# Kernel tuning notes

Measured on AMD Instinct MI355X. Metric: run time of the kernel, lower is better.

The kernel has to match this reference:

```python
import jax, jax.numpy as jnp
import numpy as np

NEG_SLOPE_ATT = 0.2   # GATConv attention leaky relu
NEG_SLOPE_ACT = 0.01  # F.leaky_relu default between layers


def gat_conv(x, src, dst, W, att_src, att_dst, bias, num_nodes):
    """PyG GATConv (concat=True, self-loops already in src/dst, no dropout at eval)."""
    H, C = att_src.shape
    h = (x @ W).reshape(num_nodes, H, C)            # [N,H,C]
    a_src = jnp.einsum('nhc,hc->nh', h, att_src)    # [N,H]
    a_dst = jnp.einsum('nhc,hc->nh', h, att_dst)
    e = jax.nn.leaky_relu(a_src[src] + a_dst[dst], NEG_SLOPE_ATT)  # [E,H]
    # segment softmax over incoming edges of each dst node
    m = jax.ops.segment_max(e, dst, num_segments=num_nodes)
    e = jnp.exp(e - m[dst])
    s = jax.ops.segment_sum(e, dst, num_segments=num_nodes)
    alpha = e / (s[dst] + 1e-16)                    # [E,H]
    msg = h[src] * alpha[..., None]                 # [E,H,C]
    out = jax.ops.segment_sum(msg, dst, num_segments=num_nodes)
    return out.reshape(num_nodes, H * C) + bias


def setup_inputs() -> dict:
    key = jax.random.key(0)
    ks = jax.random.split(key, 16)
    N, E = 50000, 1600000
    in_dim, hidden, heads, out_dim = 128, 32, 4, 64

    def glorot(k, shape):
        fan = shape[0] + shape[-1]
        return jax.random.uniform(k, shape, jnp.float32, -1.0, 1.0) * np.sqrt(6.0 / fan)

    x = jax.random.normal(ks[0], (N, in_dim), jnp.float32)
    edge_index = jax.random.randint(ks[1], (2, E), 0, N, jnp.int64)
    return {
        'x': x,
        'edge_index': edge_index,
        'W1': glorot(ks[2], (in_dim, heads * hidden)),
        'a1_src': glorot(ks[3], (heads, hidden)),
        'a1_dst': glorot(ks[4], (heads, hidden)),
        'b1': jnp.zeros((heads * hidden,), jnp.float32),
        'W2': glorot(ks[5], (heads * hidden, out_dim)),
        'a2_src': glorot(ks[6], (1, out_dim)),
        'a2_dst': glorot(ks[7], (1, out_dim)),
        'b2': jnp.zeros((out_dim,), jnp.float32),
        'Wd1': glorot(ks[8], (2 * out_dim, hidden)),
        'bd1': jnp.zeros((hidden,), jnp.float32),
        'Wd2': glorot(ks[9], (hidden, 1)),
        'bd2': jnp.zeros((1,), jnp.float32),
    }


def reference(x, edge_index, W1, a1_src, a1_dst, b1, W2, a2_src, a2_dst, b2,
              Wd1, bd1, Wd2, bd2):
    N = x.shape[0]
    # GATConv adds self-loops internally
    loops = jnp.arange(N, dtype=edge_index.dtype)
    src = jnp.concatenate([edge_index[0], loops])
    dst = jnp.concatenate([edge_index[1], loops])

    h1 = gat_conv(x, src, dst, W1, a1_src, a1_dst, b1, N)
    h1 = jax.nn.leaky_relu(h1, NEG_SLOPE_ACT)
    z = gat_conv(h1, src, dst, W2, a2_src, a2_dst, b2, N)

    # decoder: gather-concat-MLP over original edges
    feats = jnp.concatenate([z[edge_index[0]], z[edge_index[1]]], axis=1)  # [E,2*out]
    hdec = jax.nn.relu(feats @ Wd1 + bd1)
    edge_pred = hdec @ Wd2 + bd2                                           # [E,1]
    return edge_pred, z
```

## Files before the change

### kernel.cpp

```cpp
#include <hip/hip_runtime.h>
#include <hip/hip_bf16.h>
#include <math.h>

#define NEG_ATT 0.2f
#define NEG_ACT 0.01f
#define SHIFT_C 16.0f
#define CHUNK_E 8192
#define STAGE_MAX 12544

typedef __hip_bfloat16  bf16;
typedef unsigned short u16;
typedef short s8v __attribute__((ext_vector_type(8)));
typedef float f4v __attribute__((ext_vector_type(4)));

__device__ __forceinline__ float bflo(unsigned w) { return __uint_as_float(w << 16); }
__device__ __forceinline__ float bfhi(unsigned w) { return __uint_as_float(w & 0xFFFF0000u); }
__device__ __forceinline__ float lrelu_att(float a) { return fmaxf(a, NEG_ATT * a); }
__device__ __forceinline__ u16 f2b(float v) { bf16 h = __float2bfloat16(v); return *(u16*)&h; }

template<int MODE, int K, int CT, int INBF>
__device__ __forceinline__ void mfma_body(int bx, const void* __restrict__ in_,
                                          const u16* __restrict__ Wp,
                                          const float* __restrict__ bias,
                                          bf16* __restrict__ ob, bf16* __restrict__ ob2,
                                          float* __restrict__ o1, float* __restrict__ o2, int N) {
    constexpr int KK = K / 32;
    constexpr int KP = K + 8;
    __shared__ u16 As[64][KP];
    const int tid = threadIdx.x;
    const int w = tid >> 6, lane = tid & 63;
    const int row0 = bx * 64;
    for (int i = tid; i < 64 * K; i += 256) {
        int rl = (K == 128) ? (i >> 7) : (i >> 6);
        int k  = i - rl * K;
        int n = row0 + rl;
        float v = 0.f;
        if (n < N) {
            if (INBF) v = __uint_as_float((unsigned)((const u16*)in_)[(size_t)n * K + k] << 16);
            else      v = ((const float*)in_)[(size_t)n * K + k];
        }
        if (MODE == 1) v = v > 0.f ? v : NEG_ACT * v;
        As[rl][k] = f2b(v);
    }
    __syncthreads();
    const int rloc = w * 16 + (lane & 15);
    const int kgrp = lane >> 4;
    s8v af[KK];
    #pragma unroll
    for (int kk = 0; kk < KK; ++kk)
        af[kk] = *(const s8v*)&As[rloc][kk * 32 + kgrp * 8];
    #pragma unroll
    for (int ct = 0; ct < CT; ++ct) {
        f4v acc = {0.f, 0.f, 0.f, 0.f};
        #pragma unroll
        for (int kk = 0; kk < KK; ++kk) {
            s8v b = *(const s8v*)&Wp[(size_t)((ct * KK + kk) * 64 + lane) * 8];
            acc = __builtin_amdgcn_mfma_f32_16x16x32_bf16(af[kk], b, acc, 0, 0, 0);
        }
        const int colb = ct * 16 + (lane & 15);
        #pragma unroll
        for (int r = 0; r < 4; ++r) {
            int n = row0 + w * 16 + kgrp * 4 + r;
            if (n >= N) continue;
            float val = acc[r];
            if (MODE == 0) {
                if (colb < 128)      ob[(size_t)n * 128 + colb] = __float2bfloat16(val);
                else if (colb < 132) o1[n * 4 + (colb - 128)] = val;
                else if (colb < 136) o2[n * 4 + (colb - 132)] = val;
            } else if (MODE == 1) {
                if (colb < 64)       ob[(size_t)n * 64 + colb] = __float2bfloat16(val);
                else if (colb == 64) o1[n] = val;
                else if (colb == 65) o2[n] = val;
            } else {
                if (colb < 32) ob[(size_t)n * 32 + colb] = __float2bfloat16(val + bias[colb]);
                else           ob2[(size_t)n * 32 + (colb - 32)] = __float2bfloat16(val);
            }
        }
    }
}

template<int MODE, int K, int CT, int INBF>
__global__ void k_mfma(const void* __restrict__ in_, const u16* __restrict__ Wp,
                       const float* __restrict__ bias,
                       bf16* __restrict__ ob, bf16* __restrict__ ob2,
                       float* __restrict__ o1, float* __restrict__ o2, int N) {
    mfma_body<MODE, K, CT, INBF>(blockIdx.x, in_, Wp, bias, ob, ob2, o1, o2, N);
}

__global__ void k_packz(const float* __restrict__ W1, const float* __restrict__ a1sw,
                        const float* __restrict__ a1dw,
                        const float* __restrict__ W2, const float* __restrict__ a2sw,
                        const float* __restrict__ a2dw,
                        const float* __restrict__ Wd1,
                        u16* __restrict__ Wp1, u16* __restrict__ Wp2, u16* __restrict__ Wpd,
                        int* __restrict__ bhist) {
    if (blockIdx.x == 48) {
        if (threadIdx.x < 257) bhist[threadIdx.x] = 0;
        return;
    }
    const int T1 = 9 * 4 * 64 * 8, T2 = 5 * 4 * 64 * 8, TD = 4 * 2 * 64 * 8;
    for (int gi = blockIdx.x * 256 + threadIdx.x; gi < T1 + T2 + TD; gi += 48 * 256) {
        if (gi < T1) {
            int i = gi;
            int ct = i >> 11, rem = i & 2047;
            int kk = rem >> 9, l = (rem >> 3) & 63, j = i & 7;
            int k = kk * 32 + ((l >> 4) << 3) + j;
            int c = ct * 16 + (l & 15);
            float v = 0.f;
            if (c < 128) v = W1[k * 128 + c];
            else if (c < 132) {
                int h = c - 128;
                for (int q = 0; q < 32; ++q) v += W1[k * 128 + h * 32 + q] * a1sw[h * 32 + q];
            } else if (c < 136) {
                int h = c - 132;
                for (int q = 0; q < 32; ++q) v += W1[k * 128 + h * 32 + q] * a1dw[h * 32 + q];
            }
            Wp1[i] = f2b(v);
        } else if (gi < T1 + T2) {
            int i = gi - T1;
            int ct = i >> 11, rem = i & 2047;
            int kk = rem >> 9, l = (rem >> 3) & 63, j = i & 7;
            int k = kk * 32 + ((l >> 4) << 3) + j;
            int c = ct * 16 + (l & 15);
            float v = 0.f;
            if (c < 64) v = W2[k * 64 + c];
            else if (c == 64) { for (int q = 0; q < 64; ++q) v += W2[k * 64 + q] * a2sw[q]; }
            else if (c == 65) { for (int q = 0; q < 64; ++q) v += W2[k * 64 + q] * a2dw[q]; }
            Wp2[i] = f2b(v);
        } else {
            int i = gi - T1 - T2;
            int ct = i >> 10, rem = i & 1023;
            int kk = rem >> 9, l = (rem >> 3) & 63, j = i & 7;
            int k = kk * 32 + ((l >> 4) << 3) + j;
            int c = ct * 16 + (l & 15);
            float v = (c < 32) ? Wd1[k * 32 + c] : Wd1[(64 + k) * 32 + (c - 32)];
            Wpd[i] = f2b(v);
        }
    }
}

__global__ void k_front(const int* __restrict__ ei, int E, int N, int* __restrict__ bhist,
                        const float* __restrict__ x, const u16* __restrict__ Wp1,
                        bf16* __restrict__ h1b, float* __restrict__ a1s, float* __restrict__ a1d) {
    if (blockIdx.x < 512) {
        __shared__ int h[256];
        h[threadIdx.x] = 0;
        __syncthreads();
        const long E2 = (long)E + N;
        for (long e = (long)blockIdx.x * 256 + threadIdx.x; e < E2; e += 512L * 256) {
            int d = (e < E) ? ei[E + e] : (int)(e - E);
            atomicAdd(&h[d >> 8], 1);
        }
        __syncthreads();
        if (h[threadIdx.x]) atomicAdd(&bhist[threadIdx.x], h[threadIdx.x]);
    } else {
        mfma_body<0, 128, 9, 0>(blockIdx.x - 512, x, Wp1, nullptr, h1b, h1b, a1s, a1d, N);
    }
}

__global__ void k_scanA(const int* __restrict__ bhist, int NBKT, int total,
                        int* __restrict__ bbase, int* __restrict__ bcur,
                        int* __restrict__ rowptr, int N) {
    __shared__ int ps[256];
    const int t = threadIdx.x;
    int v = (t < NBKT) ? bhist[t] : 0;
    ps[t] = v;
    __syncthreads();
    for (int off = 1; off < 256; off <<= 1) {
        int u = (t >= off) ? ps[t - off] : 0;
        __syncthreads();
        ps[t] += u;
        __syncthreads();
    }
    int ex = ps[t] - v;
    if (t < NBKT) { bbase[t] = ex; bcur[t] = ex; }
    if (t == 0) { bbase[NBKT] = total; rowptr[N] = total; }
}

__global__ void k_scatterA(const int* __restrict__ ei, int E, int N,
                           int* __restrict__ bcur, unsigned* __restrict__ pk) {
    __shared__ int cnt[256], offs[256], cur[256], gpos[256], ps[256];
    const int tid = threadIdx.x;
    const long E2 = (long)E + N;
    const long chunk0 = (long)blockIdx.x * CHUNK_E;
    const int cmax = (int)min((long)CHUNK_E, E2 - chunk0);
    cnt[tid] = 0;
    __syncthreads();
    for (int i = tid; i < cmax; i += 256) {
        long e = chunk0 + i;
        int d = (e < E) ? ei[E + e] : (int)(e - E);
        atomicAdd(&cnt[d >> 8], 1);
    }
    __syncthreads();
    int v = cnt[tid];
    ps[tid] = v;
    __syncthreads();
    for (int off = 1; off < 256; off <<= 1) {
        int u = (tid >= off) ? ps[tid - off] : 0;
        __syncthreads();
        ps[tid] += u;
        __syncthreads();
    }
    offs[tid] = ps[tid] - v;
    cur[tid]  = ps[tid] - v;
    gpos[tid] = atomicAdd(&bcur[tid], v);
    __syncthreads();
    for (int i = tid; i < cmax; i += 256) {
        long e = chunk0 + i;
        int d, s;
        if (e < E) { d = ei[E + e]; s = ei[e]; } else { d = s = (int)(e - E); }
        int b = d >> 8;
        int r = atomicAdd(&cur[b], 1);
        pk[gpos[b] + (r - offs[b])] = ((unsigned)(d & 255) << 16) | (unsigned)s;
    }
}

__global__ void k_scatterB(const unsigned* __restrict__ pk, const int* __restrict__ bbase,
                           int N, int* __restrict__ rowptr, u16* __restrict__ col) {
    __shared__ int hist[256], loff[256], lcur[256], ps[256];
    __shared__ u16 stage[STAGE_MAX];
    const int b = blockIdx.x;
    const int tid = threadIdx.x;
    const int ebeg = bbase[b], eend = bbase[b + 1];
    const int cnt = eend - ebeg;
    hist[tid] = 0;
    __syncthreads();
    for (int i = tid; i < cnt; i += 256) {
        unsigned p = pk[ebeg + i];
        atomicAdd(&hist[(p >> 16) & 255], 1);
    }
    __syncthreads();
    int v = hist[tid];
    ps[tid] = v;
    __syncthreads();
    for (int off = 1; off < 256; off <<= 1) {
        int u = (tid >= off) ? ps[tid - off] : 0;
        __syncthreads();
        ps[tid] += u;
        __syncthreads();
    }
    loff[tid] = ps[tid] - v;
    lcur[tid] = ps[tid] - v;
    const int n0 = b << 8;
    if (n0 + tid < N) rowptr[n0 + tid] = ebeg + loff[tid];
    __syncthreads();
    if (cnt <= STAGE_MAX) {
        for (int i = tid; i < cnt; i += 256) {
            unsigned p = pk[ebeg + i];
            int r = atomicAdd(&lcur[(p >> 16) & 255], 1);
            stage[r] = (u16)(p & 0xFFFFu);
        }
        __syncthreads();
        for (int i = tid; i < cnt; i += 256) col[ebeg + i] = stage[i];
    } else {
        for (int i = tid; i < cnt; i += 256) {
            unsigned p = pk[ebeg + i];
            int r = atomicAdd(&lcur[(p >> 16) & 255], 1);
            col[ebeg + r] = (u16)(p & 0xFFFFu);
        }
    }
}

__global__ void k_aggr1(const int* __restrict__ rowptr, const u16* __restrict__ col,
                        const unsigned* __restrict__ h1q, const float* __restrict__ a1s,
                        const float* __restrict__ a1d, const float* __restrict__ b1,
                        unsigned* __restrict__ g1b, int N) {
    __shared__ float als[4][64][4];
    __shared__ int   scol[4][64];
    const int w = threadIdx.x >> 6;
    const int lane = threadIdx.x & 63;
    const int d = blockIdx.x * 4 + w;
    if (d >= N) return;
    const int lo = rowptr[d], hi = rowptr[d + 1];
    const float4 ad4 = *(const float4*)&a1d[d * 4];

    const int hh = lane >> 4;
    float acc0 = 0.f, acc1 = 0.f;
    float ws0 = 0.f, ws1 = 0.f, ws2 = 0.f, ws3 = 0.f;
    for (int base = lo; base < hi; base += 64) {
        const int cnt = min(64, hi - base);
        if (lane < cnt) {
            int s = col[base + lane];
            float4 as4 = *(const float4*)&a1s[s * 4];
            float a0 = lrelu_att(as4.x + ad4.x) - SHIFT_C;
            float a1 = lrelu_att(as4.y + ad4.y) - SHIFT_C;
            float a2 = lrelu_att(as4.z + ad4.z) - SHIFT_C;
            float a3 = lrelu_att(as4.w + ad4.w) - SHIFT_C;
            float4 al;
            al.x = __expf(a0); al.y = __expf(a1);
            al.z = __expf(a2); al.w = __expf(a3);
            ws0 += al.x; ws1 += al.y; ws2 += al.z; ws3 += al.w;
            *(float4*)&als[w][lane][0] = al;
            scol[w][lane] = s;
        }
        __builtin_amdgcn_wave_barrier();
        int t = 0;
        for (; t + 8 <= cnt; t += 8) {
            unsigned vv[8];
            float aa[8];
            #pragma unroll
            for (int q = 0; q < 8; ++q) {
                int s = scol[w][t + q];
                vv[q] = h1q[(((unsigned)s) << 6) | (unsigned)lane];
                aa[q] = als[w][t + q][hh];
            }
            #pragma unroll
            for (int q = 0; q < 8; ++q) {
                acc0 = fmaf(bflo(vv[q]), aa[q], acc0);
                acc1 = fmaf(bfhi(vv[q]), aa[q], acc1);
            }
        }
        for (; t < cnt; ++t) {
            int s = scol[w][t];
            float al = als[w][t][hh];
            unsigned v = h1q[(((unsigned)s) << 6) | (unsigned)lane];
            acc0 = fmaf(bflo(v), al, acc0);
            acc1 = fmaf(bfhi(v), al, acc1);
        }
        __builtin_amdgcn_wave_barrier();
    }
    #pragma unroll
    for (int off = 32; off >= 1; off >>= 1) {
        ws0 += __shfl_xor(ws0, off);
        ws1 += __shfl_xor(ws1, off);
        ws2 += __shfl_xor(ws2, off);
        ws3 += __shfl_xor(ws3, off);
    }
    float wsel = (hh == 0) ? ws0 : (hh == 1) ? ws1 : (hh == 2) ? ws2 : ws3;
    float inv = 1.f / (wsel + 1e-16f);
    unsigned outw = ((unsigned)f2b(acc1 * inv + b1[2 * lane + 1]) << 16)
                  | (unsigned)f2b(acc0 * inv + b1[2 * lane]);
    g1b[(size_t)d * 64 + lane] = outw;
}

__global__ void k_aggr2(const int* __restrict__ rowptr, const u16* __restrict__ col,
                        const unsigned short* __restrict__ h2s, const float* __restrict__ a2s,
                        const float* __restrict__ a2d, const float* __restrict__ b2,
                        float* __restrict__ zout, int N) {
    __shared__ float als[4][64];
    __shared__ int   scol[4][64];
    const int w = threadIdx.x >> 6;
    const int lane = threadIdx.x & 63;
    const int d = blockIdx.x * 4 + w;
    if (d >= N) return;
    const int lo = rowptr[d], hi = rowptr[d + 1];
    const float ad = a2d[d];

    float acc = 0.f, wsum = 0.f;
    for (int base = lo; base < hi; base += 64) {
        const int cnt = min(64, hi - base);
        if (lane < cnt) {
            int s = col[base + lane];
            float a = lrelu_att(a2s[s] + ad) - SHIFT_C;
            float al = __expf(a);
            wsum += al;
            als[w][lane] = al;
            scol[w][lane] = s;
        }
        __builtin_amdgcn_wave_barrier();
        int t = 0;
        for (; t + 8 <= cnt; t += 8) {
            float vv[8], aa[8];
            #pragma unroll
            for (int q = 0; q < 8; ++q) {
                int s = scol[w][t + q];
                vv[q] = __uint_as_float((unsigned)h2s[(((unsigned)s) << 6) | (unsigned)lane] << 16);
                aa[q] = als[w][t + q];
            }
            #pragma unroll
            for (int q = 0; q < 8; ++q) acc = fmaf(vv[q], aa[q], acc);
        }
        for (; t < cnt; ++t) {
            int s = scol[w][t];
            float v = __uint_as_float((unsigned)h2s[(((unsigned)s) << 6) | (unsigned)lane] << 16);
            acc = fmaf(v, als[w][t], acc);
        }
        __builtin_amdgcn_wave_barrier();
    }
    #pragma unroll
    for (int off = 32; off >= 1; off >>= 1) wsum += __shfl_xor(wsum, off);
    zout[(long)d * 64 + lane] = acc / (wsum + 1e-16f) + b2[lane];
}

__global__ void k_dec2(const int* __restrict__ ei, int E,
                       const bf16* __restrict__ u, const bf16* __restrict__ v,
                       const float* __restrict__ Wd2, const float* __restrict__ bd2,
                       float* __restrict__ pred) {
    const int g = threadIdx.x >> 3;
    const int l = threadIdx.x & 7;
    long e0 = (long)blockIdx.x * 64 + g * 2;
    if (e0 >= E) return;
    long e1 = e0 + 1;
    const bool has1 = (e1 < E);
    int s0 = ei[e0], d0 = ei[E + e0];
    int s1 = has1 ? (int)ei[e1] : s0;
    int d1 = has1 ? (int)ei[E + e1] : d0;
    uint2 ua0 = *(const uint2*)(u + (long)s0 * 32 + l * 4);
    uint2 vb0 = *(const uint2*)(v + (long)d0 * 32 + l * 4);
    uint2 ua1 = *(const uint2*)(u + (long)s1 * 32 + l * 4);
    uint2 vb1 = *(const uint2*)(v + (long)d1 * 32 + l * 4);
    float4 wv = *(const float4*)&Wd2[l * 4];
    float p0, p1;
    {
        float h0 = fmaxf(bflo(ua0.x) + bflo(vb0.x), 0.f);
        float h1 = fmaxf(bfhi(ua0.x) + bfhi(vb0.x), 0.f);
        float h2 = fmaxf(bflo(ua0.y) + bflo(vb0.y), 0.f);
        float h3 = fmaxf(bfhi(ua0.y) + bfhi(vb0.y), 0.f);
        p0 = h0 * wv.x;
        p0 = fmaf(h1, wv.y, p0);
        p0 = fmaf(h2, wv.z, p0);
        p0 = fmaf(h3, wv.w, p0);
    }
    {
        float h0 = fmaxf(bflo(ua1.x) + bflo(vb1.x), 0.f);
        float h1 = fmaxf(bfhi(ua1.x) + bfhi(vb1.x), 0.f);
        float h2 = fmaxf(bflo(ua1.y) + bflo(vb1.y), 0.f);
        float h3 = fmaxf(bfhi(ua1.y) + bfhi(vb1.y), 0.f);
        p1 = h0 * wv.x;
        p1 = fmaf(h1, wv.y, p1);
        p1 = fmaf(h2, wv.z, p1);
        p1 = fmaf(h3, wv.w, p1);
    }
    p0 += __shfl_xor(p0, 1, 8);
    p0 += __shfl_xor(p0, 2, 8);
    p0 += __shfl_xor(p0, 4, 8);
    p1 += __shfl_xor(p1, 1, 8);
    p1 += __shfl_xor(p1, 2, 8);
    p1 += __shfl_xor(p1, 4, 8);
    if (l == 0) {
        pred[e0] = p0 + bd2[0];
        if (has1) pred[e1] = p1 + bd2[0];
    }
}

extern "C" void kernel_launch(void* const* d_in, const int* in_sizes, int n_in,
                              void* d_out, int out_size, void* d_ws, size_t ws_size,
                              hipStream_t stream) {
    const float* x    = (const float*)d_in[0];
    const int*   ei   = (const int*)d_in[1];
    const float* W1   = (const float*)d_in[2];
    const float* a1sw = (const float*)d_in[3];
    const float* a1dw = (const float*)d_in[4];
    const float* b1   = (const float*)d_in[5];
    const float* W2   = (const float*)d_in[6];
    const float* a2sw = (const float*)d_in[7];
    const float* a2dw = (const float*)d_in[8];
    const float* b2   = (const float*)d_in[9];
    const float* Wd1  = (const float*)d_in[10];
    const float* bd1  = (const float*)d_in[11];
    const float* Wd2  = (const float*)d_in[12];
    const float* bd2  = (const float*)d_in[13];

    const int N = in_sizes[0] / 128;
    const int E = in_sizes[1] / 2;
    const int E2 = E + N;
    const int NBKT = (N + 255) >> 8;

    float* pred = (float*)d_out;
    float* zout = (float*)d_out + E;

    float* W = (float*)d_ws;
    size_t o = 0;
    unsigned* g1b = (unsigned*)(W + o); o += (size_t)N * 64;
    bf16* h1b  = (bf16*)(W + o); o += (size_t)N * 64;
    bf16* h2b  = (bf16*)(W + o); o += (size_t)N * 32;
    bf16* ub   = (bf16*)(W + o); o += (size_t)N * 16;
    bf16* vb   = (bf16*)(W + o); o += (size_t)N * 16;
    float* a1s = W + o; o += (size_t)N * 4;
    float* a1d = W + o; o += (size_t)N * 4;
    float* a2s = W + o; o += (size_t)N;
    float* a2d = W + o; o += (size_t)N;
    int* rowptr = (int*)(W + o); o += (size_t)N + 1;
    unsigned* pk = (unsigned*)(W + o); o += (size_t)E2;
    u16* col    = (u16*)(W + o); o += ((size_t)E2 + 1) / 2;
    int* bhist  = (int*)(W + o); o += 257;
    int* bbase  = (int*)(W + o); o += 257;
    int* bcur   = (int*)(W + o); o += 257;
    u16* Wp1   = (u16*)(W + o); o += 9216;
    u16* Wp2   = (u16*)(W + o); o += 5120;
    u16* Wpd   = (u16*)(W + o); o += 2048;
    if (ws_size < o * sizeof(float)) return;

    const int TB = 256;
    const int NBLK = (N + 63) >> 6;

    k_packz<<<49, TB, 0, stream>>>(W1, a1sw, a1dw, W2, a2sw, a2dw, Wd1, Wp1, Wp2, Wpd, bhist);
    k_front<<<512 + NBLK, TB, 0, stream>>>(ei, E, N, bhist, x, Wp1, h1b, a1s, a1d);
    k_scanA<<<1, TB, 0, stream>>>(bhist, NBKT, E2, bbase, bcur, rowptr, N);
    k_scatterA<<<(E2 + CHUNK_E - 1) / CHUNK_E, TB, 0, stream>>>(ei, E, N, bcur, pk);
    k_scatterB<<<NBKT, TB, 0, stream>>>(pk, bbase, N, rowptr, col);
    k_aggr1<<<(N + 3) / 4, TB, 0, stream>>>(rowptr, col, (const unsigned*)h1b, a1s, a1d, b1, g1b, N);
    k_mfma<1, 128, 5, 1><<<NBLK, TB, 0, stream>>>(g1b, Wp2, bd1, h2b, h2b, a2s, a2d, N);
    k_aggr2<<<(N + 3) / 4, TB, 0, stream>>>(rowptr, col, (const unsigned short*)h2b, a2s, a2d, b2, zout, N);
    k_mfma<2, 64, 4, 0><<<NBLK, TB, 0, stream>>>(zout, Wpd, bd1, ub, vb, a1s, a1d, N);
    k_dec2<<<(E + 63) / 64, TB, 0, stream>>>(ei, E, ub, vb, Wd2, bd2, pred);
}
```

Baseline: 239.4 us.

## Fuse GAT aggregation kernels with following MFMA projection GEMMs

Merges the layer-1 aggregation with the layer-2 projection GEMM, and the layer-2 aggregation with the decoder projection GEMM. Each block aggregates 64 nodes into shared memory and then runs MFMA on them. This removes the g1b intermediate buffer, the zout re-read and two kernel launches. The cost is far fewer blocks, each wave processing 16 nodes serially, which reduces parallelism and latency hiding for the irregular gathers.

```diff
diff --git a/kernel.cpp b/kernel.cpp
--- a/kernel.cpp
+++ b/kernel.cpp
@@ -18,43 +18,32 @@
 __device__ __forceinline__ float lrelu_att(float a) { return fmaxf(a, NEG_ATT * a); }
 __device__ __forceinline__ u16 f2b(float v) { bf16 h = __float2bfloat16(v); return *(u16*)&h; }
 
-template<int MODE, int K, int CT, int INBF>
-__device__ __forceinline__ void mfma_body(int bx, const void* __restrict__ in_,
-                                          const u16* __restrict__ Wp,
-                                          const float* __restrict__ bias,
-                                          bf16* __restrict__ ob, bf16* __restrict__ ob2,
-                                          float* __restrict__ o1, float* __restrict__ o2, int N) {
-    constexpr int KK = K / 32;
-    constexpr int KP = K + 8;
-    __shared__ u16 As[64][KP];
+__device__ __forceinline__ void gemm1_body(int bx, const float* __restrict__ in,
+                                           const u16* __restrict__ Wp,
+                                           bf16* __restrict__ ob,
+                                           float* __restrict__ o1, float* __restrict__ o2, int N) {
+    __shared__ u16 As[64][136];
     const int tid = threadIdx.x;
     const int w = tid >> 6, lane = tid & 63;
     const int row0 = bx * 64;
-    for (int i = tid; i < 64 * K; i += 256) {
-        int rl = (K == 128) ? (i >> 7) : (i >> 6);
-        int k  = i - rl * K;
+    for (int i = tid; i < 64 * 128; i += 256) {
+        int rl = i >> 7, k = i & 127;
         int n = row0 + rl;
-        float v = 0.f;
-        if (n < N) {
-            if (INBF) v = __uint_as_float((unsigned)((const u16*)in_)[(size_t)n * K + k] << 16);
-            else      v = ((const float*)in_)[(size_t)n * K + k];
-        }
-        if (MODE == 1) v = v > 0.f ? v : NEG_ACT * v;
-        As[rl][k] = f2b(v);
+        As[rl][k] = f2b((n < N) ? in[(size_t)n * 128 + k] : 0.f);
     }
     __syncthreads();
     const int rloc = w * 16 + (lane & 15);
     const int kgrp = lane >> 4;
-    s8v af[KK];
+    s8v af[4];
     #pragma unroll
-    for (int kk = 0; kk < KK; ++kk)
+    for (int kk = 0; kk < 4; ++kk)
         af[kk] = *(const s8v*)&As[rloc][kk * 32 + kgrp * 8];
     #pragma unroll
-    for (int ct = 0; ct < CT; ++ct) {
+    for (int ct = 0; ct < 9; ++ct) {
         f4v acc = {0.f, 0.f, 0.f, 0.f};
         #pragma unroll
-        for (int kk = 0; kk < KK; ++kk) {
-            s8v b = *(const s8v*)&Wp[(size_t)((ct * KK + kk) * 64 + lane) * 8];
+        for (int kk = 0; kk < 4; ++kk) {
+            s8v b = *(const s8v*)&Wp[(size_t)((ct * 4 + kk) * 64 + lane) * 8];
             acc = __builtin_amdgcn_mfma_f32_16x16x32_bf16(af[kk], b, acc, 0, 0, 0);
         }
         const int colb = ct * 16 + (lane & 15);
@@ -63,28 +52,11 @@
             int n = row0 + w * 16 + kgrp * 4 + r;
             if (n >= N) continue;
             float val = acc[r];
-            if (MODE == 0) {
-                if (colb < 128)      ob[(size_t)n * 128 + colb] = __float2bfloat16(val);
-                else if (colb < 132) o1[n * 4 + (colb - 128)] = val;
-                else if (colb < 136) o2[n * 4 + (colb - 132)] = val;
-            } else if (MODE == 1) {
-                if (colb < 64)       ob[(size_t)n * 64 + colb] = __float2bfloat16(val);
-                else if (colb == 64) o1[n] = val;
-                else if (colb == 65) o2[n] = val;
-            } else {
-                if (colb < 32) ob[(size_t)n * 32 + colb] = __float2bfloat16(val + bias[colb]);
-                else           ob2[(size_t)n * 32 + (colb - 32)] = __float2bfloat16(val);
-            }
-        }
-    }
-}
-
-template<int MODE, int K, int CT, int INBF>
-__global__ void k_mfma(const void* __restrict__ in_, const u16* __restrict__ Wp,
-                       const float* __restrict__ bias,
-                       bf16* __restrict__ ob, bf16* __restrict__ ob2,
-                       float* __restrict__ o1, float* __restrict__ o2, int N) {
-    mfma_body<MODE, K, CT, INBF>(blockIdx.x, in_, Wp, bias, ob, ob2, o1, o2, N);
+            if (colb < 128)      ob[(size_t)n * 128 + colb] = __float2bfloat16(val);
+            else if (colb < 132) o1[n * 4 + (colb - 128)] = val;
+            else if (colb < 136) o2[n * 4 + (colb - 132)] = val;
+        }
+    }
 }
 
 __global__ void k_packz(const float* __restrict__ W1, const float* __restrict__ a1sw,
@@ -154,7 +126,7 @@
         __syncthreads();
         if (h[threadIdx.x]) atomicAdd(&bhist[threadIdx.x], h[threadIdx.x]);
     } else {
-        mfma_body<0, 128, 9, 0>(blockIdx.x - 512, x, Wp1, nullptr, h1b, h1b, a1s, a1d, N);
+        gemm1_body(blockIdx.x - 512, x, Wp1, h1b, a1s, a1d, N);
     }
 }
 
@@ -261,125 +233,194 @@
     }
 }
 
-__global__ void k_aggr1(const int* __restrict__ rowptr, const u16* __restrict__ col,
-                        const unsigned* __restrict__ h1q, const float* __restrict__ a1s,
-                        const float* __restrict__ a1d, const float* __restrict__ b1,
-                        unsigned* __restrict__ g1b, int N) {
+__global__ void k_l1(const int* __restrict__ rowptr, const u16* __restrict__ col,
+                     const unsigned* __restrict__ h1q, const float* __restrict__ a1s,
+                     const float* __restrict__ a1d, const float* __restrict__ b1,
+                     const u16* __restrict__ Wp2,
+                     bf16* __restrict__ h2b, float* __restrict__ a2s, float* __restrict__ a2d,
+                     int N) {
+    __shared__ u16 As[64][136];
     __shared__ float als[4][64][4];
     __shared__ int   scol[4][64];
-    const int w = threadIdx.x >> 6;
-    const int lane = threadIdx.x & 63;
-    const int d = blockIdx.x * 4 + w;
-    if (d >= N) return;
-    const int lo = rowptr[d], hi = rowptr[d + 1];
-    const float4 ad4 = *(const float4*)&a1d[d * 4];
-
+    const int tid = threadIdx.x;
+    const int w = tid >> 6, lane = tid & 63;
+    const int n0 = blockIdx.x * 64;
     const int hh = lane >> 4;
-    float acc0 = 0.f, acc1 = 0.f;
-    float ws0 = 0.f, ws1 = 0.f, ws2 = 0.f, ws3 = 0.f;
-    for (int base = lo; base < hi; base += 64) {
-        const int cnt = min(64, hi - base);
-        if (lane < cnt) {
-            int s = col[base + lane];
-            float4 as4 = *(const float4*)&a1s[s * 4];
-            float a0 = lrelu_att(as4.x + ad4.x) - SHIFT_C;
-            float a1 = lrelu_att(as4.y + ad4.y) - SHIFT_C;
-            float a2 = lrelu_att(as4.z + ad4.z) - SHIFT_C;
-            float a3 = lrelu_att(as4.w + ad4.w) - SHIFT_C;
-            float4 al;
-            al.x = __expf(a0); al.y = __expf(a1);
-            al.z = __expf(a2); al.w = __expf(a3);
-            ws0 += al.x; ws1 += al.y; ws2 += al.z; ws3 += al.w;
-            *(float4*)&als[w][lane][0] = al;
-            scol[w][lane] = s;
-        }
-        __builtin_amdgcn_wave_barrier();
-        int t = 0;
-        for (; t + 8 <= cnt; t += 8) {
-            unsigned vv[8];
-            float aa[8];
-            #pragma unroll
-            for (int q = 0; q < 8; ++q) {
-                int s = scol[w][t + q];
-                vv[q] = h1q[(((unsigned)s) << 6) | (unsigned)lane];
-                aa[q] = als[w][t + q][hh];
-            }
-            #pragma unroll
-            for (int q = 0; q < 8; ++q) {
-                acc0 = fmaf(bflo(vv[q]), aa[q], acc0);
-                acc1 = fmaf(bfhi(vv[q]), aa[q], acc1);
-            }
-        }
-        for (; t < cnt; ++t) {
-            int s = scol[w][t];
-            float al = als[w][t][hh];
-            unsigned v = h1q[(((unsigned)s) << 6) | (unsigned)lane];
-            acc0 = fmaf(bflo(v), al, acc0);
-            acc1 = fmaf(bfhi(v), al, acc1);
-        }
-        __builtin_amdgcn_wave_barrier();
-    }
+
+    for (int sub = 0; sub < 16; ++sub) {
+        const int dl = w * 16 + sub;
+        const int d = n0 + dl;
+        if (d >= N) { *(unsigned*)&As[dl][2 * lane] = 0; continue; }
+        const int lo = rowptr[d], hi = rowptr[d + 1];
+        const float4 ad4 = *(const float4*)&a1d[d * 4];
+        float acc0 = 0.f, acc1 = 0.f;
+        float ws0 = 0.f, ws1 = 0.f, ws2 = 0.f, ws3 = 0.f;
+        for (int base = lo; base < hi; base += 64) {
+            const int cnt = min(64, hi - base);
+            if (lane < cnt) {
+                int s = col[base + lane];
+                float4 as4 = *(const float4*)&a1s[s * 4];
+                float a0 = lrelu_att(as4.x + ad4.x) - SHIFT_C;
+                float a1 = lrelu_att(as4.y + ad4.y) - SHIFT_C;
+                float a2 = lrelu_att(as4.z + ad4.z) - SHIFT_C;
+                float a3 = lrelu_att(as4.w + ad4.w) - SHIFT_C;
+                float4 al;
+                al.x = __expf(a0); al.y = __expf(a1);
+                al.z = __expf(a2); al.w = __expf(a3);
+                ws0 += al.x; ws1 += al.y; ws2 += al.z; ws3 += al.w;
+                *(float4*)&als[w][lane][0] = al;
+                scol[w][lane] = s;
+            }
+            __builtin_amdgcn_wave_barrier();
+            int t = 0;
+            for (; t + 8 <= cnt; t += 8) {
+                unsigned vv[8];
+                float aa[8];
+                #pragma unroll
+                for (int q = 0; q < 8; ++q) {
+                    int s = scol[w][t + q];
+                    vv[q] = h1q[(((unsigned)s) << 6) | (unsigned)lane];
+                    aa[q] = als[w][t + q][hh];
+                }
+                #pragma unroll
+                for (int q = 0; q < 8; ++q) {
+                    acc0 = fmaf(bflo(vv[q]), aa[q], acc0);
+                    acc1 = fmaf(bfhi(vv[q]), aa[q], acc1);
+                }
+            }
+            for (; t < cnt; ++t) {
+                int s = scol[w][t];
+                float al = als[w][t][hh];
+                unsigned v = h1q[(((unsigned)s) << 6) | (unsigned)lane];
+                acc0 = fmaf(bflo(v), al, acc0);
+                acc1 = fmaf(bfhi(v), al, acc1);
+            }
+            __builtin_amdgcn_wave_barrier();
+        }
+        #pragma unroll
+        for (int off = 32; off >= 1; off >>= 1) {
+            ws0 += __shfl_xor(ws0, off);
+            ws1 += __shfl_xor(ws1, off);
+            ws2 += __shfl_xor(ws2, off);
+            ws3 += __shfl_xor(ws3, off);
+        }
+        float wsel = (hh == 0) ? ws0 : (hh == 1) ? ws1 : (hh == 2) ? ws2 : ws3;
+        float inv = 1.f / (wsel + 1e-16f);
+        float g0 = acc0 * inv + b1[2 * lane];
+        float g1v = acc1 * inv + b1[2 * lane + 1];
+        g0  = g0  > 0.f ? g0  : NEG_ACT * g0;
+        g1v = g1v > 0.f ? g1v : NEG_ACT * g1v;
+        *(unsigned*)&As[dl][2 * lane] = ((unsigned)f2b(g1v) << 16) | (unsigned)f2b(g0);
+    }
+    __syncthreads();
+    const int rloc = w * 16 + (lane & 15);
+    const int kgrp = lane >> 4;
+    s8v af[4];
     #pragma unroll
-    for (int off = 32; off >= 1; off >>= 1) {
-        ws0 += __shfl_xor(ws0, off);
-        ws1 += __shfl_xor(ws1, off);
-        ws2 += __shfl_xor(ws2, off);
-        ws3 += __shfl_xor(ws3, off);
-    }
-    float wsel = (hh == 0) ? ws0 : (hh == 1) ? ws1 : (hh == 2) ? ws2 : ws3;
-    float inv = 1.f / (wsel + 1e-16f);
-    unsigned outw = ((unsigned)f2b(acc1 * inv + b1[2 * lane + 1]) << 16)
-                  | (unsigned)f2b(acc0 * inv + b1[2 * lane]);
-    g1b[(size_t)d * 64 + lane] = outw;
-}
-
-__global__ void k_aggr2(const int* __restrict__ rowptr, const u16* __restrict__ col,
-                        const unsigned short* __restrict__ h2s, const float* __restrict__ a2s,
-                        const float* __restrict__ a2d, const float* __restrict__ b2,
-                        float* __restrict__ zout, int N) {
+    for (int kk = 0; kk < 4; ++kk)
+        af[kk] = *(const s8v*)&As[rloc][kk * 32 + kgrp * 8];
+    #pragma unroll
+    for (int ct = 0; ct < 5; ++ct) {
+        f4v acc = {0.f, 0.f, 0.f, 0.f};
+        #pragma unroll
+        for (int kk = 0; kk < 4; ++kk) {
+            s8v b = *(const s8v*)&Wp2[(size_t)((ct * 4 + kk) * 64 + lane) * 8];
+            acc = __builtin_amdgcn_mfma_f32_16x16x32_bf16(af[kk], b, acc, 0, 0, 0);
+        }
+        const int colb = ct * 16 + (lane & 15);
+        #pragma unroll
+        for (int r = 0; r < 4; ++r) {
+            int n = n0 + w * 16 + kgrp * 4 + r;
+            if (n >= N) continue;
+            float val = acc[r];
+            if (colb < 64)       h2b[(size_t)n * 64 + colb] = __float2bfloat16(val);
+            else if (colb == 64) a2s[n] = val;
+            else if (colb == 65) a2d[n] = val;
+        }
+    }
+}
+
+__global__ void k_l2(const int* __restrict__ rowptr, const u16* __restrict__ col,
+                     const unsigned short* __restrict__ h2s, const float* __restrict__ a2s,
+                     const float* __restrict__ a2d, const float* __restrict__ b2,
+                     const u16* __restrict__ Wpd, const float* __restrict__ bd1,
+                     float* __restrict__ zout, bf16* __restrict__ ub, bf16* __restrict__ vb,
+                     int N) {
+    __shared__ u16 As[64][72];
     __shared__ float als[4][64];
     __shared__ int   scol[4][64];
-    const int w = threadIdx.x >> 6;
-    const int lane = threadIdx.x & 63;
-    const int d = blockIdx.x * 4 + w;
-    if (d >= N) return;
-    const int lo = rowptr[d], hi = rowptr[d + 1];
-    const float ad = a2d[d];
-
-    float acc = 0.f, wsum = 0.f;
-    for (int base = lo; base < hi; base += 64) {
-        const int cnt = min(64, hi - base);
-        if (lane < cnt) {
-            int s = col[base + lane];
-            float a = lrelu_att(a2s[s] + ad) - SHIFT_C;
-            float al = __expf(a);
-            wsum += al;
-            als[w][lane] = al;
-            scol[w][lane] = s;
-        }
-        __builtin_amdgcn_wave_barrier();
-        int t = 0;
-        for (; t + 8 <= cnt; t += 8) {
-            float vv[8], aa[8];
-            #pragma unroll
-            for (int q = 0; q < 8; ++q) {
-                int s = scol[w][t + q];
-                vv[q] = __uint_as_float((unsigned)h2s[(((unsigned)s) << 6) | (unsigned)lane] << 16);
-                aa[q] = als[w][t + q];
-            }
-            #pragma unroll
-            for (int q = 0; q < 8; ++q) acc = fmaf(vv[q], aa[q], acc);
-        }
-        for (; t < cnt; ++t) {
-            int s = scol[w][t];
-            float v = __uint_as_float((unsigned)h2s[(((unsigned)s) << 6) | (unsigned)lane] << 16);
-            acc = fmaf(v, als[w][t], acc);
-        }
-        __builtin_amdgcn_wave_barrier();
-    }
+    const int tid = threadIdx.x;
+    const int w = tid >> 6, lane = tid & 63;
+    const int n0 = blockIdx.x * 64;
+
+    for (int sub = 0; sub < 16; ++sub) {
+        const int dl = w * 16 + sub;
+        const int d = n0 + dl;
+        if (d >= N) { As[dl][lane] = 0; continue; }
+        const int lo = rowptr[d], hi = rowptr[d + 1];
+        const float ad = a2d[d];
+        float acc = 0.f, wsum = 0.f;
+        for (int base = lo; base < hi; base += 64) {
+            const int cnt = min(64, hi - base);
+            if (lane < cnt) {
+                int s = col[base + lane];
+                float a = lrelu_att(a2s[s] + ad) - SHIFT_C;
+                float al = __expf(a);
+                wsum += al;
+                als[w][lane] = al;
+                scol[w][lane] = s;
+            }
+            __builtin_amdgcn_wave_barrier();
+            int t = 0;
+            for (; t + 8 <= cnt; t += 8) {
+                float vv[8], aa[8];
+                #pragma unroll
+                for (int q = 0; q < 8; ++q) {
+                    int s = scol[w][t + q];
+                    vv[q] = __uint_as_float((unsigned)h2s[(((unsigned)s) << 6) | (unsigned)lane] << 16);
+                    aa[q] = als[w][t + q];
+                }
+                #pragma unroll
+                for (int q = 0; q < 8; ++q) acc = fmaf(vv[q], aa[q], acc);
+            }
+            for (; t < cnt; ++t) {
+                int s = scol[w][t];
+                float v = __uint_as_float((unsigned)h2s[(((unsigned)s) << 6) | (unsigned)lane] << 16);
+                acc = fmaf(v, als[w][t], acc);
+            }
+            __builtin_amdgcn_wave_barrier();
+        }
+        #pragma unroll
+        for (int off = 32; off >= 1; off >>= 1) wsum += __shfl_xor(wsum, off);
+        float val = acc / (wsum + 1e-16f) + b2[lane];
+        zout[(long)d * 64 + lane] = val;
+        As[dl][lane] = f2b(val);
+    }
+    __syncthreads();
+    const int rloc = w * 16 + (lane & 15);
+    const int kgrp = lane >> 4;
+    s8v af[2];
     #pragma unroll
-    for (int off = 32; off >= 1; off >>= 1) wsum += __shfl_xor(wsum, off);
-    zout[(long)d * 64 + lane] = acc / (wsum + 1e-16f) + b2[lane];
+    for (int kk = 0; kk < 2; ++kk)
+        af[kk] = *(const s8v*)&As[rloc][kk * 32 + kgrp * 8];
+    #pragma unroll
+    for (int ct = 0; ct < 4; ++ct) {
+        f4v acc = {0.f, 0.f, 0.f, 0.f};
+        #pragma unroll
+        for (int kk = 0; kk < 2; ++kk) {
+            s8v b = *(const s8v*)&Wpd[(size_t)((ct * 2 + kk) * 64 + lane) * 8];
+            acc = __builtin_amdgcn_mfma_f32_16x16x32_bf16(af[kk], b, acc, 0, 0, 0);
+        }
+        const int colb = ct * 16 + (lane & 15);
+        #pragma unroll
+        for (int r = 0; r < 4; ++r) {
+            int n = n0 + w * 16 + kgrp * 4 + r;
+            if (n >= N) continue;
+            float val = acc[r];
+            if (colb < 32) ub[(size_t)n * 32 + colb] = __float2bfloat16(val + bd1[colb]);
+            else           vb[(size_t)n * 32 + (colb - 32)] = __float2bfloat16(val);
+        }
+    }
 }
 
 __global__ void k_dec2(const int* __restrict__ ei, int E,
@@ -461,7 +502,6 @@
 
     float* W = (float*)d_ws;
     size_t o = 0;
-    unsigned* g1b = (unsigned*)(W + o); o += (size_t)N * 64;
     bf16* h1b  = (bf16*)(W + o); o += (size_t)N * 64;
     bf16* h2b  = (bf16*)(W + o); o += (size_t)N * 32;
     bf16* ub   = (bf16*)(W + o); o += (size_t)N * 16;
@@ -489,9 +529,9 @@
     k_scanA<<<1, TB, 0, stream>>>(bhist, NBKT, E2, bbase, bcur, rowptr, N);
     k_scatterA<<<(E2 + CHUNK_E - 1) / CHUNK_E, TB, 0, stream>>>(ei, E, N, bcur, pk);
     k_scatterB<<<NBKT, TB, 0, stream>>>(pk, bbase, N, rowptr, col);
-    k_aggr1<<<(N + 3) / 4, TB, 0, stream>>>(rowptr, col, (const unsigned*)h1b, a1s, a1d, b1, g1b, N);
-    k_mfma<1, 128, 5, 1><<<NBLK, TB, 0, stream>>>(g1b, Wp2, bd1, h2b, h2b, a2s, a2d, N);
-    k_aggr2<<<(N + 3) / 4, TB, 0, stream>>>(rowptr, col, (const unsigned short*)h2b, a2s, a2d, b2, zout, N);
-    k_mfma<2, 64, 4, 0><<<NBLK, TB, 0, stream>>>(zout, Wpd, bd1, ub, vb, a1s, a1d, N);
+    k_l1<<<NBLK, TB, 0, stream>>>(rowptr, col, (const unsigned*)h1b, a1s, a1d, b1,
+                                  Wp2, h2b, a2s, a2d, N);
+    k_l2<<<NBLK, TB, 0, stream>>>(rowptr, col, (const unsigned short*)h2b, a2s, a2d, b2,
+                                  Wpd, bd1, zout, ub, vb, N);
     k_dec2<<<(E + 63) / 64, TB, 0, stream>>>(ei, E, ub, vb, Wd2, bd2, pred);
 }
```

New measurement: 278.6 us. 1.16x slower.
